# Kernel tuning notes

Hardware: AMD Instinct MI355X
Metric: run time of the kernel (lower is better)

The kernel has to match this reference:

```python
import jax, jax.numpy as jnp
import numpy as np

EPS = 1.1920929e-07  # torch.finfo(float32).eps
TOP_K = 2
AUX_COEF = 0.01

def rmsnorm(x):
    return x * jax.lax.rsqrt(jnp.mean(x * x, axis=-1, keepdims=True) + EPS)

def setup_inputs() -> dict:
    key = jax.random.key(0)
    ks = jax.random.split(key, 8)
    B, T, C, H, E = 1, 2048, 1024, 2048, 8
    x = jax.random.normal(ks[0], (B, T, C), jnp.float32)
    gate_w = jax.random.normal(ks[1], (E, C), jnp.float32) * 0.02
    w1 = jax.random.normal(ks[2], (E, H, C), jnp.float32) * 0.02  # expert up-proj
    w2 = jax.random.normal(ks[3], (E, C, H), jnp.float32) * 0.02  # expert down-proj
    shared_gate_w = jax.random.normal(ks[4], (1, C), jnp.float32) * 0.02
    k_w = jax.random.normal(ks[5], (H, C), jnp.float32) * 0.02
    k_b = jax.random.normal(ks[6], (H,), jnp.float32) * 0.01
    v_w = jax.random.normal(ks[7], (C, H), jnp.float32) * 0.02
    v_b = jnp.zeros((C,), jnp.float32)
    return dict(x=x, gate_w=gate_w, w1=w1, w2=w2, shared_gate_w=shared_gate_w,
                k_w=k_w, k_b=k_b, v_w=v_w, v_b=v_b)

def reference(x, gate_w, w1, w2, shared_gate_w, k_w, k_b, v_w, v_b):
    B, T, C = x.shape
    xt = rmsnorm(x.reshape(-1, C))                     # [N,C]
    N = xt.shape[0]
    raw = xt @ gate_w.T                                # [N,E]
    scores = jax.nn.softmax(raw, axis=-1)
    topk_w, topk_idx = jax.lax.top_k(scores, TOP_K)    # [N,k]
    topk_w = topk_w / (jnp.sum(topk_w, axis=-1, keepdims=True) + 1e-6)
    E = scores.shape[-1]
    rows = jnp.arange(N)[:, None]
    onehot = jnp.zeros_like(scores).at[rows, topk_idx].set(1.0 / TOP_K)
    aux_loss = E * jnp.sum(jnp.mean(onehot, 0) * jnp.mean(scores, 0)) * AUX_COEF
    # dense gate matrix [N,E]: combine weight per (token, expert)
    g = jnp.zeros_like(scores).at[rows, topk_idx].add(topk_w)
    # grouped-GEMM expressed densely over experts (reference math identical)
    h = jnp.einsum('nc,ehc->neh', xt, w1)              # [N,E,H]
    h = jnp.square(jax.nn.relu(h)) * g[:, :, None]     # act + gate-combine weight
    out = jnp.einsum('neh,ech->nc', h, w2)             # [N,C]
    # shared expert: sigmoid gate * MLP (MLP re-norms its input)
    sg = jax.nn.sigmoid(xt @ shared_gate_w.T)          # [N,1]
    xs = rmsnorm(xt)
    kk = jnp.square(jax.nn.relu(xs @ k_w.T + k_b))     # [N,H]
    shared = kk @ v_w.T + v_b                          # [N,C]
    out = out + sg * shared
    return out.reshape(B, T, C), aux_loss
```

## Files before the change

kernel.cpp:

```cpp
#include <hip/hip_runtime.h>
#include <hip/hip_bf16.h>
#include <stdint.h>

typedef __bf16 bf16;
typedef bf16 bf16x8 __attribute__((ext_vector_type(8)));
typedef bf16 bf16x4 __attribute__((ext_vector_type(4)));
typedef float f32x4 __attribute__((ext_vector_type(4)));

constexpr int N = 2048;
constexpr int C = 1024;
constexpr int H = 2048;
constexpr int E = 8;
constexpr float EPS = 1.1920929e-07f;

constexpr int BM = 128, BN = 256;
constexpr int GT = 32;
constexpr int ASUB = 128 * 64;
constexpr int BSUB = 256 * 64;

constexpr int PREP_GATE = N / GT;
constexpr int PREP_RMS  = N;
constexpr int CVT_BLK   = ((E * H * C + H * C) / 4) / 1024;
constexpr int PREP_TOTAL = PREP_GATE + PREP_RMS + 2 * CVT_BLK;

constexpr int P1_UP    = E * (N / BM) * (H / BN);
constexpr int P1_KP    = (N / BM) * (H / BN);
constexpr int P1_TOTAL = P1_UP + P1_KP;

constexpr int P2_DOWN  = (E * 2) * (N / BM) * (C / BN);
constexpr int P2_VP    = (N / BM) * (C / BN) * 2;
constexpr int P2_TOTAL = P2_DOWN + P2_VP;

constexpr int COMBINE_BLK = (N * C / 4) / 256;

__device__ __forceinline__ void cvt_pair(const float* __restrict__ s1, bf16* __restrict__ d1,
                                         size_t n1, const float* __restrict__ s2,
                                         bf16* __restrict__ d2, int cbx) {
  size_t base = (size_t)cbx * 1024 + threadIdx.x;
  #pragma unroll
  for (int j = 0; j < 4; ++j) {
    size_t i = base + (size_t)j * 256;
    if (i < n1) {
      float4 v = ((const float4*)s1)[i];
      bf16x4 o = { (bf16)v.x, (bf16)v.y, (bf16)v.z, (bf16)v.w };
      ((bf16x4*)d1)[i] = o;
    } else {
      size_t k = i - n1;
      float4 v = ((const float4*)s2)[k];
      bf16x4 o = { (bf16)v.x, (bf16)v.y, (bf16)v.z, (bf16)v.w };
      ((bf16x4*)d2)[k] = o;
    }
  }
}

__global__ __launch_bounds__(256) void prep_kernel(
    const float* __restrict__ x, const float* __restrict__ gate_w,
    const float* __restrict__ sgw, const float* __restrict__ w1,
    const float* __restrict__ kw, const float* __restrict__ w2,
    const float* __restrict__ vw,
    bf16* __restrict__ xtb, float* __restrict__ rs2_arr,
    float* __restrict__ g, float* __restrict__ sgbuf,
    int* __restrict__ counts, int* __restrict__ lists,
    float* __restrict__ scoresums,
    bf16* __restrict__ w1b, bf16* __restrict__ kwb,
    bf16* __restrict__ w2b, bf16* __restrict__ vwb) {
  __shared__ float wsm[9][1024];
  __shared__ float s_scores[8];
  __shared__ int   s_cnt[8];
  __shared__ int   s_base[8];
  __shared__ int   s_e1[GT], s_p1[GT], s_e2[GT], s_p2[GT];
  const int bx = blockIdx.x;
  const int tid = threadIdx.x, lane = tid & 63, wave = tid >> 6;

  if (bx >= PREP_GATE + PREP_RMS + CVT_BLK) {
    cvt_pair(w2, w2b, (size_t)E * C * H / 4, vw, vwb,
             bx - PREP_GATE - PREP_RMS - CVT_BLK);
    return;
  }
  if (bx >= PREP_GATE + PREP_RMS) {
    cvt_pair(w1, w1b, (size_t)E * H * C / 4, kw, kwb, bx - PREP_GATE - PREP_RMS);
    return;
  }
  if (bx >= PREP_GATE) {
    int n = bx - PREP_GATE;
    float4 v = ((const float4*)(x + (size_t)n * C))[tid];
    float ss = v.x*v.x + v.y*v.y + v.z*v.z + v.w*v.w;
    #pragma unroll
    for (int off = 32; off > 0; off >>= 1) ss += __shfl_down(ss, off, 64);
    __shared__ float red[4];
    __shared__ float tot;
    if (lane == 0) red[wave] = ss;
    __syncthreads();
    if (tid == 0) tot = red[0] + red[1] + red[2] + red[3];
    __syncthreads();
    float sumsq = tot;
    float rs1 = rsqrtf(sumsq * (1.f / C) + EPS);
    bf16x4 o = { (bf16)(v.x*rs1), (bf16)(v.y*rs1), (bf16)(v.z*rs1), (bf16)(v.w*rs1) };
    ((bf16x4*)(xtb + (size_t)n * C))[tid] = o;
    if (tid == 0) {
      float m2 = sumsq * rs1 * rs1 * (1.f / C);
      rs2_arr[n] = rsqrtf(m2 + EPS);
    }
    return;
  }
  for (int i = tid; i < 9 * 1024; i += 256) {
    int e = i >> 10, c = i & 1023;
    wsm[e][c] = (e < 8) ? gate_w[i] : sgw[c];
  }
  if (tid < 8) { s_scores[tid] = 0.f; s_cnt[tid] = 0; }
  __syncthreads();

  const int tok0 = bx * GT + wave * (GT / 4);
  for (int tt = 0; tt < GT / 4; ++tt) {
    const int tok = tok0 + tt;
    const float* xr = x + (size_t)tok * C;
    float acc[10];
    #pragma unroll
    for (int e = 0; e < 10; e++) acc[e] = 0.f;
    #pragma unroll
    for (int k = 0; k < 16; ++k) {
      int c = k * 64 + lane;
      float xv = xr[c];
      #pragma unroll
      for (int e = 0; e < 9; e++) acc[e] = fmaf(xv, wsm[e][c], acc[e]);
      acc[9] = fmaf(xv, xv, acc[9]);
    }
    #pragma unroll
    for (int e = 0; e < 10; e++) {
      float v = acc[e];
      #pragma unroll
      for (int off = 32; off > 0; off >>= 1) v += __shfl_xor(v, off, 64);
      acc[e] = v;
    }
    if (lane == 0) {
      float rs1 = rsqrtf(acc[9] * (1.f / C) + EPS);
      float raw[9];
      #pragma unroll
      for (int e = 0; e < 9; e++) raw[e] = acc[e] * rs1;
      float m = raw[0];
      for (int e = 1; e < 8; e++) m = fmaxf(m, raw[e]);
      float sc[8], s = 0.f;
      for (int e = 0; e < 8; e++) { sc[e] = expf(raw[e] - m); s += sc[e]; }
      float inv = 1.f / s;
      for (int e = 0; e < 8; e++) sc[e] *= inv;
      int i1 = 0;
      for (int e = 1; e < 8; e++) if (sc[e] > sc[i1]) i1 = e;
      int i2 = -1;
      for (int e = 0; e < 8; e++) {
        if (e == i1) continue;
        if (i2 < 0 || sc[e] > sc[i2]) i2 = e;
      }
      float denom = sc[i1] + sc[i2] + 1e-6f;
      float* gr = g + (size_t)tok * E;
      #pragma unroll
      for (int e = 0; e < 8; e++) gr[e] = 0.f;
      gr[i1] = sc[i1] / denom;
      gr[i2] = sc[i2] / denom;
      sgbuf[tok] = 1.f / (1.f + expf(-raw[8]));
      for (int e = 0; e < 8; e++) atomicAdd(&s_scores[e], sc[e]);
      int lt = wave * (GT / 4) + tt;
      int p1 = atomicAdd(&s_cnt[i1], 1);
      int p2 = atomicAdd(&s_cnt[i2], 1);
      s_e1[lt] = i1; s_p1[lt] = p1;
      s_e2[lt] = i2; s_p2[lt] = p2;
    }
  }
  __syncthreads();
  if (tid < 8) {
    s_base[tid] = atomicAdd(&counts[tid], s_cnt[tid]);
    atomicAdd(&scoresums[tid], s_scores[tid]);
  }
  __syncthreads();
  if (tid < GT) {
    int tok = bx * GT + tid;
    int e1 = s_e1[tid], e2 = s_e2[tid];
    lists[e1 * N + s_base[e1] + s_p1[tid]] = (tok << 1);
    lists[e2 * N + s_base[e2] + s_p2[tid]] = (tok << 1) | 1;
  }
}

#define GLL(gp, lp)                                                             \
  __builtin_amdgcn_global_load_lds((__attribute__((address_space(1))) void*)(gp), \
                                   (__attribute__((address_space(3))) void*)(lp), 16, 0, 0)

__device__ __forceinline__ void mfma_loop(
    const char* pA, const char* pB0, const char* pB1,
    char* As, char* Bs, int dA, int dB0, int dB1,
    int lane, int kIters, int mb, int nb, f32x4 acc[4][4]) {
  const int arow = lane & 15;
  const int koff = (lane >> 4) * 16;
  for (int kt = 0; kt < kIters; ++kt) {
    GLL(pA,       As + dA);          GLL(pA  + 64, As + ASUB + dA);
    GLL(pB0,      Bs + dB0);         GLL(pB0 + 64, Bs + BSUB + dB0);
    GLL(pB1,      Bs + dB1);         GLL(pB1 + 64, Bs + BSUB + dB1);
    pA += 128; pB0 += 128; pB1 += 128;
    __syncthreads();
    #pragma unroll
    for (int kh = 0; kh < 2; ++kh) {
      const char* Ac = As + kh * ASUB;
      const char* Bc = Bs + kh * BSUB;
      bf16x8 a[4], b[4];
      #pragma unroll
      for (int i = 0; i < 4; ++i) {
        a[i] = *(const bf16x8*)(Ac + (mb + i * 16 + arow) * 64 + koff);
        b[i] = *(const bf16x8*)(Bc + (nb + i * 16 + arow) * 64 + koff);
      }
      #pragma unroll
      for (int i = 0; i < 4; ++i)
        #pragma unroll
        for (int j = 0; j < 4; ++j)
          acc[i][j] = __builtin_amdgcn_mfma_f32_16x16x32_bf16(a[i], b[j], acc[i][j], 0, 0, 0);
    }
    __syncthreads();
  }
}

#define GEMM_VARS                                                  \
  const int tid = threadIdx.x;                                     \
  const int lane = tid & 63, wave = tid >> 6;            \
  const int mb = (wave >> 2) * 64, nb = (wave & 3) * 64;           \
  const int srow = wave * 16 + (lane >> 2);       \
  const int scb = (lane & 3) * 16;              \
  const int dA  = wave * 1024;                      \
  const int dB0 = wave * 1024;                                     \
  const int dB1 = 8192 + wave * 1024;                              \
  const int col = lane & 15, quad = lane >> 4;                     \
  f32x4 acc[4][4] = {};

__device__ __forceinline__ void run_up(
    const bf16* __restrict__ xtb, const bf16* __restrict__ w1b,
    const float* __restrict__ g, const int* __restrict__ lists,
    const int* __restrict__ counts, bf16* __restrict__ hb,
    int e, int m0, int h0, char* As, char* Bs, int* toks) {
  const int cnt = counts[e];
  if (m0 >= cnt) return;
  GEMM_VARS
  if (tid < BM) toks[tid] = lists[e * N + min(m0 + tid, cnt - 1)];
  __syncthreads();
  const char* pA  = (const char*)xtb + ((size_t)(toks[srow] >> 1) * C) * 2 + scb;
  const char* pB0 = (const char*)w1b + ((size_t)e * H * C + (size_t)(h0 + srow) * C) * 2 + scb;
  const char* pB1 = (const char*)w1b + ((size_t)e * H * C + (size_t)(h0 + 128 + srow) * C) * 2 + scb;
  mfma_loop(pA, pB0, pB1, As, Bs, dA, dB0, dB1, lane, C / 64, mb, nb, acc);
  #pragma unroll
  for (int mi = 0; mi < 4; mi++) {
    #pragma unroll
    for (int r = 0; r < 4; r++) {
      int ml = mb + mi * 16 + quad * 4 + r;
      if (m0 + ml < cnt) {
        int packed = toks[ml];
        float gv = g[(size_t)(packed >> 1) * E + e];
        size_t base = (size_t)packed * H + h0 + nb;
        #pragma unroll
        for (int ni = 0; ni < 4; ni++) {
          float v = fmaxf(acc[mi][ni][r], 0.f);
          hb[base + ni * 16 + col] = (bf16)(v * v * gv);
        }
      }
    }
  }
}

__device__ __forceinline__ void run_kproj(
    const bf16* __restrict__ xtb, const bf16* __restrict__ kwb,
    const float* __restrict__ rs2, const float* __restrict__ k_b,
    bf16* __restrict__ kkb, int n0, int h0, char* As, char* Bs) {
  GEMM_VARS
  const char* pA  = (const char*)xtb + ((size_t)(n0 + srow) * C) * 2 + scb;
  const char* pB0 = (const char*)kwb + ((size_t)(h0 + srow) * C) * 2 + scb;
  const char* pB1 = (const char*)kwb + ((size_t)(h0 + 128 + srow) * C) * 2 + scb;
  mfma_loop(pA, pB0, pB1, As, Bs, dA, dB0, dB1, lane, C / 64, mb, nb, acc);
  #pragma unroll
  for (int mi = 0; mi < 4; mi++) {
    #pragma unroll
    for (int r = 0; r < 4; r++) {
      int n = n0 + mb + mi * 16 + quad * 4 + r;
      float rs = rs2[n];
      #pragma unroll
      for (int ni = 0; ni < 4; ni++) {
        int h = h0 + nb + ni * 16 + col;
        float v = fmaf(acc[mi][ni][r], rs, k_b[h]);
        v = fmaxf(v, 0.f);
        kkb[(size_t)n * H + h] = (bf16)(v * v);
      }
    }
  }
}

__device__ __forceinline__ void run_down(
    const bf16* __restrict__ hb, const bf16* __restrict__ w2b,
    const int* __restrict__ lists, const int* __restrict__ counts,
    float* __restrict__ dp, int e, int ks, int m0, int c0,
    char* As, char* Bs, int* toks) {
  const int cnt = counts[e];
  if (m0 >= cnt) return;
  GEMM_VARS
  if (tid < BM) toks[tid] = lists[e * N + min(m0 + tid, cnt - 1)];
  __syncthreads();
  const size_t kofs = (size_t)ks * (H / 2) * 2;
  const char* pA  = (const char*)hb + ((size_t)toks[srow] * H) * 2 + kofs + scb;
  const char* pB0 = (const char*)w2b + ((size_t)e * C * H + (size_t)(c0 + srow) * H) * 2 + kofs + scb;
  const char* pB1 = (const char*)w2b + ((size_t)e * C * H + (size_t)(c0 + 128 + srow) * H) * 2 + kofs + scb;
  mfma_loop(pA, pB0, pB1, As, Bs, dA, dB0, dB1, lane, (H / 2) / 64, mb, nb, acc);
  #pragma unroll
  for (int mi = 0; mi < 4; mi++) {
    #pragma unroll
    for (int r = 0; r < 4; r++) {
      int ml = mb + mi * 16 + quad * 4 + r;
      if (m0 + ml < cnt) {
        int packed = toks[ml];
        int tok = packed >> 1, par = packed & 1;
        float* orow = dp + (((size_t)(ks * 2 + par) * N + tok) * C) + c0 + nb;
        #pragma unroll
        for (int ni = 0; ni < 4; ni++) orow[ni * 16 + col] = acc[mi][ni][r];
      }
    }
  }
}

__device__ __forceinline__ void run_vproj(
    const bf16* __restrict__ kkb, const bf16* __restrict__ vwb,
    float* __restrict__ vp, int n0, int c0, int ks, char* As, char* Bs) {
  GEMM_VARS
  const size_t kofs = (size_t)ks * (H / 2) * 2;
  const char* pA  = (const char*)kkb + ((size_t)(n0 + srow) * H) * 2 + kofs + scb;
  const char* pB0 = (const char*)vwb + ((size_t)(c0 + srow) * H) * 2 + kofs + scb;
  const char* pB1 = (const char*)vwb + ((size_t)(c0 + 128 + srow) * H) * 2 + kofs + scb;
  mfma_loop(pA, pB0, pB1, As, Bs, dA, dB0, dB1, lane, (H / 2) / 64, mb, nb, acc);
  #pragma unroll
  for (int mi = 0; mi < 4; mi++) {
    #pragma unroll
    for (int r = 0; r < 4; r++) {
      int n = n0 + mb + mi * 16 + quad * 4 + r;
      float* orow = vp + ((size_t)ks * N + n) * C + c0 + nb;
      #pragma unroll
      for (int ni = 0; ni < 4; ni++) orow[ni * 16 + col] = acc[mi][ni][r];
    }
  }
}

__global__ __launch_bounds__(512) void phase1_kernel(
    const bf16* __restrict__ xtb, const bf16* __restrict__ w1b,
    const float* __restrict__ g, const int* __restrict__ lists,
    const int* __restrict__ counts, bf16* __restrict__ hb,
    const bf16* __restrict__ kwb, const float* __restrict__ rs2,
    const float* __restrict__ k_b, bf16* __restrict__ kkb) {
  __shared__ __align__(16) char As[2 * ASUB];
  __shared__ __align__(16) char Bs[2 * BSUB];
  __shared__ int toks[BM];
  const int bx = blockIdx.x;
  if (bx < P1_UP) {
    int e = bx >> 7, rem = bx & 127;
    int h0 = (rem & 7) * BN, m0 = (rem >> 3) * BM;
    run_up(xtb, w1b, g, lists, counts, hb, e, m0, h0, As, Bs, toks);
  } else {
    int rem = bx - P1_UP;
    int n0 = (rem & 15) * BM, h0 = (rem >> 4) * BN;
    run_kproj(xtb, kwb, rs2, k_b, kkb, n0, h0, As, Bs);
  }
}

__global__ __launch_bounds__(512) void phase2_kernel(
    const bf16* __restrict__ hb, const bf16* __restrict__ w2b,
    const int* __restrict__ lists, const int* __restrict__ counts,
    const bf16* __restrict__ kkb, const bf16* __restrict__ vwb,
    float* __restrict__ dp, float* __restrict__ vp) {
  __shared__ __align__(16) char As[2 * ASUB];
  __shared__ __align__(16) char Bs[2 * BSUB];
  __shared__ int toks[BM];
  const int bx = blockIdx.x;
  if (bx < P2_DOWN) {
    int z = bx >> 6, rem = bx & 63;
    int e = z >> 1, ks = z & 1;
    int c0 = (rem & 3) * BN, m0 = (rem >> 2) * BM;
    run_down(hb, w2b, lists, counts, dp, e, ks, m0, c0, As, Bs, toks);
  } else {
    int rem = bx - P2_DOWN;
    int ks = rem >> 6, r2 = rem & 63;
    int n0 = (r2 & 15) * BM, c0 = (r2 >> 4) * BN;
    run_vproj(kkb, vwb, vp, n0, c0, ks, As, Bs);
  }
}

__global__ __launch_bounds__(256) void combine_kernel(
    const float* __restrict__ dp, const float* __restrict__ vp,
    const float* __restrict__ v_b, const float* __restrict__ sg,
    float* __restrict__ out) {
  constexpr size_t NC = (size_t)N * C;
  size_t i = (size_t)blockIdx.x * 256 + threadIdx.x;
  size_t off = i * 4;
  int n = (int)(off >> 10);
  int c = (int)(off & 1023);
  float4 a = ((const float4*)(dp))[i];
  float4 b = ((const float4*)(dp + NC))[i];
  float4 d2 = ((const float4*)(dp + 2 * NC))[i];
  float4 d3 = ((const float4*)(dp + 3 * NC))[i];
  float4 u = ((const float4*)(vp))[i];
  float4 w = ((const float4*)(vp + NC))[i];
  float4 bias = *(const float4*)(v_b + c);
  float s = sg[n];
  float4 o;
  o.x = a.x + b.x + d2.x + d3.x + s * (u.x + w.x + bias.x);
  o.y = a.y + b.y + d2.y + d3.y + s * (u.y + w.y + bias.y);
  o.z = a.z + b.z + d2.z + d3.z + s * (u.z + w.z + bias.z);
  o.w = a.w + b.w + d2.w + d3.w + s * (u.w + w.w + bias.w);
  ((float4*)out)[i] = o;
}

__global__ void aux_kernel(const float* __restrict__ scoresums,
                           const int* __restrict__ counts,
                           float* __restrict__ out_aux) {
  if (threadIdx.x == 0) {
    float a = 0.f;
    for (int e = 0; e < 8; e++)
      a += (0.5f * (float)counts[e] * (1.f / N)) * (scoresums[e] * (1.f / N));
    out_aux[0] = 8.f * a * 0.01f;
  }
}

extern "C" void kernel_launch(void* const* d_in, const int* in_sizes, int n_in,
                              void* d_out, int out_size, void* d_ws, size_t ws_size,
                              hipStream_t stream) {
  (void)in_sizes; (void)n_in; (void)ws_size;
  const float* x   = (const float*)d_in[0];
  const float* gw  = (const float*)d_in[1];
  const float* w1  = (const float*)d_in[2];
  const float* w2  = (const float*)d_in[3];
  const float* sgw = (const float*)d_in[4];
  const float* k_w = (const float*)d_in[5];
  const float* k_b = (const float*)d_in[6];
  const float* v_w = (const float*)d_in[7];
  const float* v_b = (const float*)d_in[8];
  float* out = (float*)d_out;

  char* p = (char*)d_ws;
  auto alloc = [&](size_t bytes) { char* r = p; p += (bytes + 255) & ~255ull; return r; };
  bf16* xtb  = (bf16*)alloc((size_t)N * C * 2);
  bf16* w1b  = (bf16*)alloc((size_t)E * H * C * 2);
  bf16* w2b  = (bf16*)alloc((size_t)E * C * H * 2);
  bf16* kwb  = (bf16*)alloc((size_t)H * C * 2);
  bf16* vwb  = (bf16*)alloc((size_t)C * H * 2);
  bf16* hb   = (bf16*)alloc((size_t)2 * N * H * 2);
  bf16* kkb  = (bf16*)alloc((size_t)N * H * 2);
  float* rs2 = (float*)alloc((size_t)N * 4);
  float* g   = (float*)alloc((size_t)N * E * 4);
  float* sg  = (float*)alloc((size_t)N * 4);
  float* scoresums = (float*)alloc(256);
  int* counts = (int*)alloc(256);
  int* lists  = (int*)alloc((size_t)E * N * 4);
  float* vp   = (float*)alloc((size_t)2 * N * C * 4);
  float* dp   = (float*)w1b;

  hipMemsetAsync(d_out, 0, (size_t)out_size * sizeof(float), stream);
  hipMemsetAsync(scoresums, 0, 512, stream);
  prep_kernel<<<PREP_TOTAL, 256, 0, stream>>>(
      x, gw, sgw, w1, k_w, w2, v_w, xtb, rs2, g, sg, counts, lists, scoresums,
      w1b, kwb, w2b, vwb);
  phase1_kernel<<<P1_TOTAL, 512, 0, stream>>>(
      xtb, w1b, g, lists, counts, hb, kwb, rs2, k_b, kkb);
  phase2_kernel<<<P2_TOTAL, 512, 0, stream>>>(
      hb, w2b, lists, counts, kkb, vwb, dp, vp);
  combine_kernel<<<COMBINE_BLK, 256, 0, stream>>>(dp, vp, v_b, sg, out);
  aux_kernel<<<1, 64, 0, stream>>>(scoresums, counts, out + (size_t)N * C);
}
```

Before: 295.0 us.

## Fuse fp32-to-bf16 weight conversion into GEMM B-tile loads

Drops the separate pass that converted all expert and shared weights to bf16 in the prep kernel. The GEMMs now load fp32 weights directly, convert them in registers and store bf16 into LDS, replacing the async global-to-LDS path for the B operand. The aux-loss kernel is merged into combine and the output memset is removed. In exchange each weight tile is re-read as fp32 by every M-tile block, which raises global traffic and register use. Moving B loads to synchronous register loads may also expose load latency, and a 3-blocks-per-CU launch bound is added.

```diff
diff --git a/kernel.cpp b/kernel.cpp
--- a/kernel.cpp
+++ b/kernel.cpp
@@ -20,8 +20,7 @@
 
 constexpr int PREP_GATE = N / GT;
 constexpr int PREP_RMS  = N;
-constexpr int CVT_BLK   = ((E * H * C + H * C) / 4) / 1024;
-constexpr int PREP_TOTAL = PREP_GATE + PREP_RMS + 2 * CVT_BLK;
+constexpr int PREP_TOTAL = PREP_GATE + PREP_RMS;
 
 constexpr int P1_UP    = E * (N / BM) * (H / BN);
 constexpr int P1_KP    = (N / BM) * (H / BN);
@@ -33,37 +32,13 @@
 
 constexpr int COMBINE_BLK = (N * C / 4) / 256;
 
-__device__ __forceinline__ void cvt_pair(const float* __restrict__ s1, bf16* __restrict__ d1,
-                                         size_t n1, const float* __restrict__ s2,
-                                         bf16* __restrict__ d2, int cbx) {
-  size_t base = (size_t)cbx * 1024 + threadIdx.x;
-  #pragma unroll
-  for (int j = 0; j < 4; ++j) {
-    size_t i = base + (size_t)j * 256;
-    if (i < n1) {
-      float4 v = ((const float4*)s1)[i];
-      bf16x4 o = { (bf16)v.x, (bf16)v.y, (bf16)v.z, (bf16)v.w };
-      ((bf16x4*)d1)[i] = o;
-    } else {
-      size_t k = i - n1;
-      float4 v = ((const float4*)s2)[k];
-      bf16x4 o = { (bf16)v.x, (bf16)v.y, (bf16)v.z, (bf16)v.w };
-      ((bf16x4*)d2)[k] = o;
-    }
-  }
-}
-
 __global__ __launch_bounds__(256) void prep_kernel(
     const float* __restrict__ x, const float* __restrict__ gate_w,
-    const float* __restrict__ sgw, const float* __restrict__ w1,
-    const float* __restrict__ kw, const float* __restrict__ w2,
-    const float* __restrict__ vw,
+    const float* __restrict__ sgw,
     bf16* __restrict__ xtb, float* __restrict__ rs2_arr,
     float* __restrict__ g, float* __restrict__ sgbuf,
     int* __restrict__ counts, int* __restrict__ lists,
-    float* __restrict__ scoresums,
-    bf16* __restrict__ w1b, bf16* __restrict__ kwb,
-    bf16* __restrict__ w2b, bf16* __restrict__ vwb) {
+    float* __restrict__ scoresums) {
   __shared__ float wsm[9][1024];
   __shared__ float s_scores[8];
   __shared__ int   s_cnt[8];
@@ -72,15 +47,6 @@
   const int bx = blockIdx.x;
   const int tid = threadIdx.x, lane = tid & 63, wave = tid >> 6;
 
-  if (bx >= PREP_GATE + PREP_RMS + CVT_BLK) {
-    cvt_pair(w2, w2b, (size_t)E * C * H / 4, vw, vwb,
-             bx - PREP_GATE - PREP_RMS - CVT_BLK);
-    return;
-  }
-  if (bx >= PREP_GATE + PREP_RMS) {
-    cvt_pair(w1, w1b, (size_t)E * H * C / 4, kw, kwb, bx - PREP_GATE - PREP_RMS);
-    return;
-  }
   if (bx >= PREP_GATE) {
     int n = bx - PREP_GATE;
     float4 v = ((const float4*)(x + (size_t)n * C))[tid];
@@ -183,17 +149,44 @@
   __builtin_amdgcn_global_load_lds((__attribute__((address_space(1))) void*)(gp), \
                                    (__attribute__((address_space(3))) void*)(lp), 16, 0, 0)
 
+__device__ __forceinline__ bf16x8 pack8(float4 a, float4 b) {
+  bf16x8 o = { (bf16)a.x, (bf16)a.y, (bf16)a.z, (bf16)a.w,
+               (bf16)b.x, (bf16)b.y, (bf16)b.z, (bf16)b.w };
+  return o;
+}
+
 __device__ __forceinline__ void mfma_loop(
-    const char* pA, const char* pB0, const char* pB1,
-    char* As, char* Bs, int dA, int dB0, int dB1,
-    int lane, int kIters, int mb, int nb, f32x4 acc[4][4]) {
+    const char* pA, const float* B0, int ldB,
+    char* As, char* Bs, int dA, int tid, int lane,
+    int kIters, int mb, int nb, f32x4 acc[4][4]) {
   const int arow = lane & 15;
   const int koff = (lane >> 4) * 16;
+  const int r0 = tid >> 2, cb = tid & 3;
+  const float* s0 = B0 + (size_t)r0 * ldB + cb * 8;
+  const float* s1 = B0 + (size_t)(r0 + 128) * ldB + cb * 8;
+  char* d00 = Bs + r0 * 64 + cb * 16;
+  char* d01 = Bs + (r0 + 128) * 64 + cb * 16;
   for (int kt = 0; kt < kIters; ++kt) {
-    GLL(pA,       As + dA);          GLL(pA  + 64, As + ASUB + dA);
-    GLL(pB0,      Bs + dB0);         GLL(pB0 + 64, Bs + BSUB + dB0);
-    GLL(pB1,      Bs + dB1);         GLL(pB1 + 64, Bs + BSUB + dB1);
-    pA += 128; pB0 += 128; pB1 += 128;
+    GLL(pA, As + dA);
+    GLL(pA + 64, As + ASUB + dA);
+    pA += 128;
+    const int kc = kt * 64;
+    {
+      float4 a0 = *(const float4*)(s0 + kc);
+      float4 a1 = *(const float4*)(s0 + kc + 4);
+      float4 b0 = *(const float4*)(s1 + kc);
+      float4 b1 = *(const float4*)(s1 + kc + 4);
+      *(bf16x8*)d00 = pack8(a0, a1);
+      *(bf16x8*)d01 = pack8(b0, b1);
+    }
+    {
+      float4 a0 = *(const float4*)(s0 + kc + 32);
+      float4 a1 = *(const float4*)(s0 + kc + 36);
+      float4 b0 = *(const float4*)(s1 + kc + 32);
+      float4 b1 = *(const float4*)(s1 + kc + 36);
+      *(bf16x8*)(d00 + BSUB) = pack8(a0, a1);
+      *(bf16x8*)(d01 + BSUB) = pack8(b0, b1);
+    }
     __syncthreads();
     #pragma unroll
     for (int kh = 0; kh < 2; ++kh) {
@@ -219,16 +212,14 @@
   const int tid = threadIdx.x;                                     \
   const int lane = tid & 63, wave = tid >> 6;            \
   const int mb = (wave >> 2) * 64, nb = (wave & 3) * 64;           \
-  const int srow = wave * 16 + (lane >> 2);       \
-  const int scb = (lane & 3) * 16;              \
-  const int dA  = wave * 1024;                      \
-  const int dB0 = wave * 1024;                                     \
-  const int dB1 = 8192 + wave * 1024;                              \
+  const int srow = wave * 16 + (lane >> 2);     \
+  const int scb = (lane & 3) * 16;             \
+  const int dA  = wave * 1024;                     \
   const int col = lane & 15, quad = lane >> 4;                     \
   f32x4 acc[4][4] = {};
 
 __device__ __forceinline__ void run_up(
-    const bf16* __restrict__ xtb, const bf16* __restrict__ w1b,
+    const bf16* __restrict__ xtb, const float* __restrict__ w1,
     const float* __restrict__ g, const int* __restrict__ lists,
     const int* __restrict__ counts, bf16* __restrict__ hb,
     int e, int m0, int h0, char* As, char* Bs, int* toks) {
@@ -237,10 +228,9 @@
   GEMM_VARS
   if (tid < BM) toks[tid] = lists[e * N + min(m0 + tid, cnt - 1)];
   __syncthreads();
-  const char* pA  = (const char*)xtb + ((size_t)(toks[srow] >> 1) * C) * 2 + scb;
-  const char* pB0 = (const char*)w1b + ((size_t)e * H * C + (size_t)(h0 + srow) * C) * 2 + scb;
-  const char* pB1 = (const char*)w1b + ((size_t)e * H * C + (size_t)(h0 + 128 + srow) * C) * 2 + scb;
-  mfma_loop(pA, pB0, pB1, As, Bs, dA, dB0, dB1, lane, C / 64, mb, nb, acc);
+  const char* pA = (const char*)xtb + ((size_t)(toks[srow] >> 1) * C) * 2 + scb;
+  const float* B0 = w1 + (size_t)e * H * C + (size_t)h0 * C;
+  mfma_loop(pA, B0, C, As, Bs, dA, tid, lane, C / 64, mb, nb, acc);
   #pragma unroll
   for (int mi = 0; mi < 4; mi++) {
     #pragma unroll
@@ -261,14 +251,13 @@
 }
 
 __device__ __forceinline__ void run_kproj(
-    const bf16* __restrict__ xtb, const bf16* __restrict__ kwb,
+    const bf16* __restrict__ xtb, const float* __restrict__ kw,
     const float* __restrict__ rs2, const float* __restrict__ k_b,
     bf16* __restrict__ kkb, int n0, int h0, char* As, char* Bs) {
   GEMM_VARS
-  const char* pA  = (const char*)xtb + ((size_t)(n0 + srow) * C) * 2 + scb;
-  const char* pB0 = (const char*)kwb + ((size_t)(h0 + srow) * C) * 2 + scb;
-  const char* pB1 = (const char*)kwb + ((size_t)(h0 + 128 + srow) * C) * 2 + scb;
-  mfma_loop(pA, pB0, pB1, As, Bs, dA, dB0, dB1, lane, C / 64, mb, nb, acc);
+  const char* pA = (const char*)xtb + ((size_t)(n0 + srow) * C) * 2 + scb;
+  const float* B0 = kw + (size_t)h0 * C;
+  mfma_loop(pA, B0, C, As, Bs, dA, tid, lane, C / 64, mb, nb, acc);
   #pragma unroll
   for (int mi = 0; mi < 4; mi++) {
     #pragma unroll
@@ -287,7 +276,7 @@
 }
 
 __device__ __forceinline__ void run_down(
-    const bf16* __restrict__ hb, const bf16* __restrict__ w2b,
+    const bf16* __restrict__ hb, const float* __restrict__ w2,
     const int* __restrict__ lists, const int* __restrict__ counts,
     float* __restrict__ dp, int e, int ks, int m0, int c0,
     char* As, char* Bs, int* toks) {
@@ -296,11 +285,9 @@
   GEMM_VARS
   if (tid < BM) toks[tid] = lists[e * N + min(m0 + tid, cnt - 1)];
   __syncthreads();
-  const size_t kofs = (size_t)ks * (H / 2) * 2;
-  const char* pA  = (const char*)hb + ((size_t)toks[srow] * H) * 2 + kofs + scb;
-  const char* pB0 = (const char*)w2b + ((size_t)e * C * H + (size_t)(c0 + srow) * H) * 2 + kofs + scb;
-  const char* pB1 = (const char*)w2b + ((size_t)e * C * H + (size_t)(c0 + 128 + srow) * H) * 2 + kofs + scb;
-  mfma_loop(pA, pB0, pB1, As, Bs, dA, dB0, dB1, lane, (H / 2) / 64, mb, nb, acc);
+  const char* pA = (const char*)hb + ((size_t)toks[srow] * H) * 2 + (size_t)ks * (H / 2) * 2 + scb;
+  const float* B0 = w2 + (size_t)e * C * H + (size_t)c0 * H + (size_t)ks * (H / 2);
+  mfma_loop(pA, B0, H, As, Bs, dA, tid, lane, (H / 2) / 64, mb, nb, acc);
   #pragma unroll
   for (int mi = 0; mi < 4; mi++) {
     #pragma unroll
@@ -318,14 +305,12 @@
 }
 
 __device__ __forceinline__ void run_vproj(
-    const bf16* __restrict__ kkb, const bf16* __restrict__ vwb,
+    const bf16* __restrict__ kkb, const float* __restrict__ vw,
     float* __restrict__ vp, int n0, int c0, int ks, char* As, char* Bs) {
   GEMM_VARS
-  const size_t kofs = (size_t)ks * (H / 2) * 2;
-  const char* pA  = (const char*)kkb + ((size_t)(n0 + srow) * H) * 2 + kofs + scb;
-  const char* pB0 = (const char*)vwb + ((size_t)(c0 + srow) * H) * 2 + kofs + scb;
-  const char* pB1 = (const char*)vwb + ((size_t)(c0 + 128 + srow) * H) * 2 + kofs + scb;
-  mfma_loop(pA, pB0, pB1, As, Bs, dA, dB0, dB1, lane, (H / 2) / 64, mb, nb, acc);
+  const char* pA = (const char*)kkb + ((size_t)(n0 + srow) * H) * 2 + (size_t)ks * (H / 2) * 2 + scb;
+  const float* B0 = vw + (size_t)c0 * H + (size_t)ks * (H / 2);
+  mfma_loop(pA, B0, H, As, Bs, dA, tid, lane, (H / 2) / 64, mb, nb, acc);
   #pragma unroll
   for (int mi = 0; mi < 4; mi++) {
     #pragma unroll
@@ -338,11 +323,11 @@
   }
 }
 
-__global__ __launch_bounds__(512) void phase1_kernel(
-    const bf16* __restrict__ xtb, const bf16* __restrict__ w1b,
+__global__ __launch_bounds__(512, 3) void phase1_kernel(
+    const bf16* __restrict__ xtb, const float* __restrict__ w1,
     const float* __restrict__ g, const int* __restrict__ lists,
     const int* __restrict__ counts, bf16* __restrict__ hb,
-    const bf16* __restrict__ kwb, const float* __restrict__ rs2,
+    const float* __restrict__ kw, const float* __restrict__ rs2,
     const float* __restrict__ k_b, bf16* __restrict__ kkb) {
   __shared__ __align__(16) char As[2 * ASUB];
   __shared__ __align__(16) char Bs[2 * BSUB];
@@ -351,18 +336,18 @@
   if (bx < P1_UP) {
     int e = bx >> 7, rem = bx & 127;
     int h0 = (rem & 7) * BN, m0 = (rem >> 3) * BM;
-    run_up(xtb, w1b, g, lists, counts, hb, e, m0, h0, As, Bs, toks);
+    run_up(xtb, w1, g, lists, counts, hb, e, m0, h0, As, Bs, toks);
   } else {
     int rem = bx - P1_UP;
     int n0 = (rem & 15) * BM, h0 = (rem >> 4) * BN;
-    run_kproj(xtb, kwb, rs2, k_b, kkb, n0, h0, As, Bs);
-  }
-}
-
-__global__ __launch_bounds__(512) void phase2_kernel(
-    const bf16* __restrict__ hb, const bf16* __restrict__ w2b,
+    run_kproj(xtb, kw, rs2, k_b, kkb, n0, h0, As, Bs);
+  }
+}
+
+__global__ __launch_bounds__(512, 3) void phase2_kernel(
+    const bf16* __restrict__ hb, const float* __restrict__ w2,
     const int* __restrict__ lists, const int* __restrict__ counts,
-    const bf16* __restrict__ kkb, const bf16* __restrict__ vwb,
+    const bf16* __restrict__ kkb, const float* __restrict__ vw,
     float* __restrict__ dp, float* __restrict__ vp) {
   __shared__ __align__(16) char As[2 * ASUB];
   __shared__ __align__(16) char Bs[2 * BSUB];
@@ -372,20 +357,27 @@
     int z = bx >> 6, rem = bx & 63;
     int e = z >> 1, ks = z & 1;
     int c0 = (rem & 3) * BN, m0 = (rem >> 2) * BM;
-    run_down(hb, w2b, lists, counts, dp, e, ks, m0, c0, As, Bs, toks);
+    run_down(hb, w2, lists, counts, dp, e, ks, m0, c0, As, Bs, toks);
   } else {
     int rem = bx - P2_DOWN;
     int ks = rem >> 6, r2 = rem & 63;
     int n0 = (r2 & 15) * BM, c0 = (r2 >> 4) * BN;
-    run_vproj(kkb, vwb, vp, n0, c0, ks, As, Bs);
+    run_vproj(kkb, vw, vp, n0, c0, ks, As, Bs);
   }
 }
 
 __global__ __launch_bounds__(256) void combine_kernel(
     const float* __restrict__ dp, const float* __restrict__ vp,
     const float* __restrict__ v_b, const float* __restrict__ sg,
+    const float* __restrict__ scoresums, const int* __restrict__ counts,
     float* __restrict__ out) {
   constexpr size_t NC = (size_t)N * C;
+  if (blockIdx.x == 0 && threadIdx.x == 0) {
+    float a = 0.f;
+    for (int e = 0; e < 8; e++)
+      a += (0.5f * (float)counts[e] * (1.f / N)) * (scoresums[e] * (1.f / N));
+    out[NC] = 8.f * a * 0.01f;
+  }
   size_t i = (size_t)blockIdx.x * 256 + threadIdx.x;
   size_t off = i * 4;
   int n = (int)(off >> 10);
@@ -406,21 +398,10 @@
   ((float4*)out)[i] = o;
 }
 
-__global__ void aux_kernel(const float* __restrict__ scoresums,
-                           const int* __restrict__ counts,
-                           float* __restrict__ out_aux) {
-  if (threadIdx.x == 0) {
-    float a = 0.f;
-    for (int e = 0; e < 8; e++)
-      a += (0.5f * (float)counts[e] * (1.f / N)) * (scoresums[e] * (1.f / N));
-    out_aux[0] = 8.f * a * 0.01f;
-  }
-}
-
 extern "C" void kernel_launch(void* const* d_in, const int* in_sizes, int n_in,
                               void* d_out, int out_size, void* d_ws, size_t ws_size,
                               hipStream_t stream) {
-  (void)in_sizes; (void)n_in; (void)ws_size;
+  (void)in_sizes; (void)n_in; (void)ws_size; (void)out_size;
   const float* x   = (const float*)d_in[0];
   const float* gw  = (const float*)d_in[1];
   const float* w1  = (const float*)d_in[2];
@@ -435,10 +416,6 @@
   char* p = (char*)d_ws;
   auto alloc = [&](size_t bytes) { char* r = p; p += (bytes + 255) & ~255ull; return r; };
   bf16* xtb  = (bf16*)alloc((size_t)N * C * 2);
-  bf16* w1b  = (bf16*)alloc((size_t)E * H * C * 2);
-  bf16* w2b  = (bf16*)alloc((size_t)E * C * H * 2);
-  bf16* kwb  = (bf16*)alloc((size_t)H * C * 2);
-  bf16* vwb  = (bf16*)alloc((size_t)C * H * 2);
   bf16* hb   = (bf16*)alloc((size_t)2 * N * H * 2);
   bf16* kkb  = (bf16*)alloc((size_t)N * H * 2);
   float* rs2 = (float*)alloc((size_t)N * 4);
@@ -448,17 +425,15 @@
   int* counts = (int*)alloc(256);
   int* lists  = (int*)alloc((size_t)E * N * 4);
   float* vp   = (float*)alloc((size_t)2 * N * C * 4);
-  float* dp   = (float*)w1b;
-
-  hipMemsetAsync(d_out, 0, (size_t)out_size * sizeof(float), stream);
+  float* dp   = (float*)alloc((size_t)4 * N * C * 4);
+
   hipMemsetAsync(scoresums, 0, 512, stream);
   prep_kernel<<<PREP_TOTAL, 256, 0, stream>>>(
-      x, gw, sgw, w1, k_w, w2, v_w, xtb, rs2, g, sg, counts, lists, scoresums,
-      w1b, kwb, w2b, vwb);
+      x, gw, sgw, xtb, rs2, g, sg, counts, lists, scoresums);
   phase1_kernel<<<P1_TOTAL, 512, 0, stream>>>(
-      xtb, w1b, g, lists, counts, hb, kwb, rs2, k_b, kkb);
+      xtb, w1, g, lists, counts, hb, k_w, rs2, k_b, kkb);
   phase2_kernel<<<P2_TOTAL, 512, 0, stream>>>(
-      hb, w2b, lists, counts, kkb, vwb, dp, vp);
-  combine_kernel<<<COMBINE_BLK, 256, 0, stream>>>(dp, vp, v_b, sg, out);
-  aux_kernel<<<1, 64, 0, stream>>>(scoresums, counts, out + (size_t)N * C);
-}
+      hb, w2, lists, counts, kkb, v_w, dp, vp);
+  combine_kernel<<<COMBINE_BLK, 256, 0, stream>>>(
+      dp, vp, v_b, sg, scoresums, counts, out);
+}
```

After: 363.0 us. 1.23x slower.

## Double-buffer GEMM LDS tiles with BK=32, drop gate LDS staging and aux launch

Applied to the files above, without the earlier changes.

The MFMA loop now runs over BK=32 slices with two LDS buffers. The next tile is loaded through global_load_lds while the current one is computed, using vmcnt waits and raw s_barrier in place of __syncthreads. The prep kernel reads gate weights straight from global memory instead of staging 36KB in LDS, and the aux-loss computation moves into combine_kernel, removing the aux launch and the output memset. Each k-step now issues fewer MFMAs per barrier, and the manual waitcnt scheme is fragile if the compiler reorders loads.

```diff
diff --git a/kernel.cpp b/kernel.cpp
--- a/kernel.cpp
+++ b/kernel.cpp
@@ -13,10 +13,10 @@
 constexpr int E = 8;
 constexpr float EPS = 1.1920929e-07f;
 
-constexpr int BM = 128, BN = 256;
+constexpr int BM = 128, BN = 256, BK = 32;
 constexpr int GT = 32;
-constexpr int ASUB = 128 * 64;
-constexpr int BSUB = 256 * 64;
+constexpr int ATILE = BM * BK * 2;
+constexpr int BTILE = BN * BK * 2;
 
 constexpr int PREP_GATE = N / GT;
 constexpr int PREP_RMS  = N;
@@ -64,11 +64,12 @@
     float* __restrict__ scoresums,
     bf16* __restrict__ w1b, bf16* __restrict__ kwb,
     bf16* __restrict__ w2b, bf16* __restrict__ vwb) {
-  __shared__ float wsm[9][1024];
   __shared__ float s_scores[8];
   __shared__ int   s_cnt[8];
   __shared__ int   s_base[8];
   __shared__ int   s_e1[GT], s_p1[GT], s_e2[GT], s_p2[GT];
+  __shared__ float red[4];
+  __shared__ float tot;
   const int bx = blockIdx.x;
   const int tid = threadIdx.x, lane = tid & 63, wave = tid >> 6;
 
@@ -87,8 +88,6 @@
     float ss = v.x*v.x + v.y*v.y + v.z*v.z + v.w*v.w;
     #pragma unroll
     for (int off = 32; off > 0; off >>= 1) ss += __shfl_down(ss, off, 64);
-    __shared__ float red[4];
-    __shared__ float tot;
     if (lane == 0) red[wave] = ss;
     __syncthreads();
     if (tid == 0) tot = red[0] + red[1] + red[2] + red[3];
@@ -103,10 +102,6 @@
     }
     return;
   }
-  for (int i = tid; i < 9 * 1024; i += 256) {
-    int e = i >> 10, c = i & 1023;
-    wsm[e][c] = (e < 8) ? gate_w[i] : sgw[c];
-  }
   if (tid < 8) { s_scores[tid] = 0.f; s_cnt[tid] = 0; }
   __syncthreads();
 
@@ -122,7 +117,8 @@
       int c = k * 64 + lane;
       float xv = xr[c];
       #pragma unroll
-      for (int e = 0; e < 9; e++) acc[e] = fmaf(xv, wsm[e][c], acc[e]);
+      for (int e = 0; e < 8; e++) acc[e] = fmaf(xv, gate_w[e * 1024 + c], acc[e]);
+      acc[8] = fmaf(xv, sgw[c], acc[8]);
       acc[9] = fmaf(xv, xv, acc[9]);
     }
     #pragma unroll
@@ -183,35 +179,46 @@
   __builtin_amdgcn_global_load_lds((__attribute__((address_space(1))) void*)(gp), \
                                    (__attribute__((address_space(3))) void*)(lp), 16, 0, 0)
 
+__device__ __forceinline__ void stage_step(
+    const char* pA, const char* pB0, const char* pB1,
+    char* Ab, char* Bb, int dA, int dB) {
+  GLL(pA, Ab + dA);
+  GLL(pB0, Bb + dB);
+  GLL(pB1, Bb + dB + 1024);
+}
+
 __device__ __forceinline__ void mfma_loop(
     const char* pA, const char* pB0, const char* pB1,
-    char* As, char* Bs, int dA, int dB0, int dB1,
-    int lane, int kIters, int mb, int nb, f32x4 acc[4][4]) {
+    char* As, char* Bs, int dA, int dB, int lane,
+    int kIters, int mb, int nb, f32x4 acc[4][4]) {
   const int arow = lane & 15;
   const int koff = (lane >> 4) * 16;
-  for (int kt = 0; kt < kIters; ++kt) {
-    GLL(pA,       As + dA);          GLL(pA  + 64, As + ASUB + dA);
-    GLL(pB0,      Bs + dB0);         GLL(pB0 + 64, Bs + BSUB + dB0);
-    GLL(pB1,      Bs + dB1);         GLL(pB1 + 64, Bs + BSUB + dB1);
-    pA += 128; pB0 += 128; pB1 += 128;
-    __syncthreads();
-    #pragma unroll
-    for (int kh = 0; kh < 2; ++kh) {
-      const char* Ac = As + kh * ASUB;
-      const char* Bc = Bs + kh * BSUB;
-      bf16x8 a[4], b[4];
-      #pragma unroll
-      for (int i = 0; i < 4; ++i) {
-        a[i] = *(const bf16x8*)(Ac + (mb + i * 16 + arow) * 64 + koff);
-        b[i] = *(const bf16x8*)(Bc + (nb + i * 16 + arow) * 64 + koff);
-      }
-      #pragma unroll
-      for (int i = 0; i < 4; ++i)
-        #pragma unroll
-        for (int j = 0; j < 4; ++j)
-          acc[i][j] = __builtin_amdgcn_mfma_f32_16x16x32_bf16(a[i], b[j], acc[i][j], 0, 0, 0);
-    }
-    __syncthreads();
+  stage_step(pA, pB0, pB1, As, Bs, dA, dB);
+  pA += 64; pB0 += 64; pB1 += 64;
+  for (int t = 0; t < kIters; ++t) {
+    if (t + 1 < kIters) {
+      stage_step(pA, pB0, pB1,
+                 As + ((t + 1) & 1) * ATILE, Bs + ((t + 1) & 1) * BTILE, dA, dB);
+      pA += 64; pB0 += 64; pB1 += 64;
+      asm volatile("s_waitcnt vmcnt(3)" ::: "memory");
+    } else {
+      asm volatile("s_waitcnt vmcnt(0)" ::: "memory");
+    }
+    __builtin_amdgcn_s_barrier();
+    const char* Ac = As + (t & 1) * ATILE;
+    const char* Bc = Bs + (t & 1) * BTILE;
+    bf16x8 a[4], b[4];
+    #pragma unroll
+    for (int i = 0; i < 4; ++i) {
+      a[i] = *(const bf16x8*)(Ac + (mb + i * 16 + arow) * 64 + koff);
+      b[i] = *(const bf16x8*)(Bc + (nb + i * 16 + arow) * 64 + koff);
+    }
+    #pragma unroll
+    for (int i = 0; i < 4; ++i)
+      #pragma unroll
+      for (int j = 0; j < 4; ++j)
+        acc[i][j] = __builtin_amdgcn_mfma_f32_16x16x32_bf16(a[i], b[j], acc[i][j], 0, 0, 0);
+    __builtin_amdgcn_s_barrier();
   }
 }
 
@@ -219,11 +226,10 @@
   const int tid = threadIdx.x;                                     \
   const int lane = tid & 63, wave = tid >> 6;            \
   const int mb = (wave >> 2) * 64, nb = (wave & 3) * 64;           \
-  const int srow = wave * 16 + (lane >> 2);       \
-  const int scb = (lane & 3) * 16;              \
-  const int dA  = wave * 1024;                      \
-  const int dB0 = wave * 1024;                                     \
-  const int dB1 = 8192 + wave * 1024;                              \
+  const int sra = wave * 16 + (lane >> 2);      \
+  const int srb = wave * 32 + (lane >> 2);      \
+  const int scb = (lane & 3) * 16;             \
+  const int dA = wave * 1024, dB = wave * 2048;                    \
   const int col = lane & 15, quad = lane >> 4;                     \
   f32x4 acc[4][4] = {};
 
@@ -237,10 +243,10 @@
   GEMM_VARS
   if (tid < BM) toks[tid] = lists[e * N + min(m0 + tid, cnt - 1)];
   __syncthreads();
-  const char* pA  = (const char*)xtb + ((size_t)(toks[srow] >> 1) * C) * 2 + scb;
-  const char* pB0 = (const char*)w1b + ((size_t)e * H * C + (size_t)(h0 + srow) * C) * 2 + scb;
-  const char* pB1 = (const char*)w1b + ((size_t)e * H * C + (size_t)(h0 + 128 + srow) * C) * 2 + scb;
-  mfma_loop(pA, pB0, pB1, As, Bs, dA, dB0, dB1, lane, C / 64, mb, nb, acc);
+  const char* pA  = (const char*)xtb + ((size_t)(toks[sra] >> 1) * C) * 2 + scb;
+  const char* pB0 = (const char*)w1b + ((size_t)e * H * C + (size_t)(h0 + srb) * C) * 2 + scb;
+  const char* pB1 = pB0 + (size_t)16 * C * 2;
+  mfma_loop(pA, pB0, pB1, As, Bs, dA, dB, lane, C / BK, mb, nb, acc);
   #pragma unroll
   for (int mi = 0; mi < 4; mi++) {
     #pragma unroll
@@ -265,10 +271,10 @@
     const float* __restrict__ rs2, const float* __restrict__ k_b,
     bf16* __restrict__ kkb, int n0, int h0, char* As, char* Bs) {
   GEMM_VARS
-  const char* pA  = (const char*)xtb + ((size_t)(n0 + srow) * C) * 2 + scb;
-  const char* pB0 = (const char*)kwb + ((size_t)(h0 + srow) * C) * 2 + scb;
-  const char* pB1 = (const char*)kwb + ((size_t)(h0 + 128 + srow) * C) * 2 + scb;
-  mfma_loop(pA, pB0, pB1, As, Bs, dA, dB0, dB1, lane, C / 64, mb, nb, acc);
+  const char* pA  = (const char*)xtb + ((size_t)(n0 + sra) * C) * 2 + scb;
+  const char* pB0 = (const char*)kwb + ((size_t)(h0 + srb) * C) * 2 + scb;
+  const char* pB1 = pB0 + (size_t)16 * C * 2;
+  mfma_loop(pA, pB0, pB1, As, Bs, dA, dB, lane, C / BK, mb, nb, acc);
   #pragma unroll
   for (int mi = 0; mi < 4; mi++) {
     #pragma unroll
@@ -297,10 +303,10 @@
   if (tid < BM) toks[tid] = lists[e * N + min(m0 + tid, cnt - 1)];
   __syncthreads();
   const size_t kofs = (size_t)ks * (H / 2) * 2;
-  const char* pA  = (const char*)hb + ((size_t)toks[srow] * H) * 2 + kofs + scb;
-  const char* pB0 = (const char*)w2b + ((size_t)e * C * H + (size_t)(c0 + srow) * H) * 2 + kofs + scb;
-  const char* pB1 = (const char*)w2b + ((size_t)e * C * H + (size_t)(c0 + 128 + srow) * H) * 2 + kofs + scb;
-  mfma_loop(pA, pB0, pB1, As, Bs, dA, dB0, dB1, lane, (H / 2) / 64, mb, nb, acc);
+  const char* pA  = (const char*)hb + ((size_t)toks[sra] * H) * 2 + kofs + scb;
+  const char* pB0 = (const char*)w2b + ((size_t)e * C * H + (size_t)(c0 + srb) * H) * 2 + kofs + scb;
+  const char* pB1 = pB0 + (size_t)16 * H * 2;
+  mfma_loop(pA, pB0, pB1, As, Bs, dA, dB, lane, (H / 2) / BK, mb, nb, acc);
   #pragma unroll
   for (int mi = 0; mi < 4; mi++) {
     #pragma unroll
@@ -322,10 +328,10 @@
     float* __restrict__ vp, int n0, int c0, int ks, char* As, char* Bs) {
   GEMM_VARS
   const size_t kofs = (size_t)ks * (H / 2) * 2;
-  const char* pA  = (const char*)kkb + ((size_t)(n0 + srow) * H) * 2 + kofs + scb;
-  const char* pB0 = (const char*)vwb + ((size_t)(c0 + srow) * H) * 2 + kofs + scb;
-  const char* pB1 = (const char*)vwb + ((size_t)(c0 + 128 + srow) * H) * 2 + kofs + scb;
-  mfma_loop(pA, pB0, pB1, As, Bs, dA, dB0, dB1, lane, (H / 2) / 64, mb, nb, acc);
+  const char* pA  = (const char*)kkb + ((size_t)(n0 + sra) * H) * 2 + kofs + scb;
+  const char* pB0 = (const char*)vwb + ((size_t)(c0 + srb) * H) * 2 + kofs + scb;
+  const char* pB1 = pB0 + (size_t)16 * H * 2;
+  mfma_loop(pA, pB0, pB1, As, Bs, dA, dB, lane, (H / 2) / BK, mb, nb, acc);
   #pragma unroll
   for (int mi = 0; mi < 4; mi++) {
     #pragma unroll
@@ -344,8 +350,8 @@
     const int* __restrict__ counts, bf16* __restrict__ hb,
     const bf16* __restrict__ kwb, const float* __restrict__ rs2,
     const float* __restrict__ k_b, bf16* __restrict__ kkb) {
-  __shared__ __align__(16) char As[2 * ASUB];
-  __shared__ __align__(16) char Bs[2 * BSUB];
+  __shared__ __align__(16) char As[2 * ATILE];
+  __shared__ __align__(16) char Bs[2 * BTILE];
   __shared__ int toks[BM];
   const int bx = blockIdx.x;
   if (bx < P1_UP) {
@@ -364,8 +370,8 @@
     const int* __restrict__ lists, const int* __restrict__ counts,
     const bf16* __restrict__ kkb, const bf16* __restrict__ vwb,
     float* __restrict__ dp, float* __restrict__ vp) {
-  __shared__ __align__(16) char As[2 * ASUB];
-  __shared__ __align__(16) char Bs[2 * BSUB];
+  __shared__ __align__(16) char As[2 * ATILE];
+  __shared__ __align__(16) char Bs[2 * BTILE];
   __shared__ int toks[BM];
   const int bx = blockIdx.x;
   if (bx < P2_DOWN) {
@@ -384,8 +390,15 @@
 __global__ __launch_bounds__(256) void combine_kernel(
     const float* __restrict__ dp, const float* __restrict__ vp,
     const float* __restrict__ v_b, const float* __restrict__ sg,
+    const float* __restrict__ scoresums, const int* __restrict__ counts,
     float* __restrict__ out) {
   constexpr size_t NC = (size_t)N * C;
+  if (blockIdx.x == 0 && threadIdx.x == 0) {
+    float a = 0.f;
+    for (int e = 0; e < 8; e++)
+      a += (0.5f * (float)counts[e] * (1.f / N)) * (scoresums[e] * (1.f / N));
+    out[NC] = 8.f * a * 0.01f;
+  }
   size_t i = (size_t)blockIdx.x * 256 + threadIdx.x;
   size_t off = i * 4;
   int n = (int)(off >> 10);
@@ -406,21 +419,10 @@
   ((float4*)out)[i] = o;
 }
 
-__global__ void aux_kernel(const float* __restrict__ scoresums,
-                           const int* __restrict__ counts,
-                           float* __restrict__ out_aux) {
-  if (threadIdx.x == 0) {
-    float a = 0.f;
-    for (int e = 0; e < 8; e++)
-      a += (0.5f * (float)counts[e] * (1.f / N)) * (scoresums[e] * (1.f / N));
-    out_aux[0] = 8.f * a * 0.01f;
-  }
-}
-
 extern "C" void kernel_launch(void* const* d_in, const int* in_sizes, int n_in,
                               void* d_out, int out_size, void* d_ws, size_t ws_size,
                               hipStream_t stream) {
-  (void)in_sizes; (void)n_in; (void)ws_size;
+  (void)in_sizes; (void)n_in; (void)ws_size; (void)out_size;
   const float* x   = (const float*)d_in[0];
   const float* gw  = (const float*)d_in[1];
   const float* w1  = (const float*)d_in[2];
@@ -450,7 +452,6 @@
   float* vp   = (float*)alloc((size_t)2 * N * C * 4);
   float* dp   = (float*)w1b;
 
-  hipMemsetAsync(d_out, 0, (size_t)out_size * sizeof(float), stream);
   hipMemsetAsync(scoresums, 0, 512, stream);
   prep_kernel<<<PREP_TOTAL, 256, 0, stream>>>(
       x, gw, sgw, w1, k_w, w2, v_w, xtb, rs2, g, sg, counts, lists, scoresums,
@@ -459,6 +460,6 @@
       xtb, w1b, g, lists, counts, hb, kwb, rs2, k_b, kkb);
   phase2_kernel<<<P2_TOTAL, 512, 0, stream>>>(
       hb, w2b, lists, counts, kkb, vwb, dp, vp);
-  combine_kernel<<<COMBINE_BLK, 256, 0, stream>>>(dp, vp, v_b, sg, out);
-  aux_kernel<<<1, 64, 0, stream>>>(scoresums, counts, out + (size_t)N * C);
-}
+  combine_kernel<<<COMBINE_BLK, 256, 0, stream>>>(
+      dp, vp, v_b, sg, scoresums, counts, out);
+}
```

After: 299.2 us. No clear change (+1.4%).
